# Optimization experiments

Measured on AMD Instinct MI355X. Metric: run time of the kernel, lower is better.

The kernel has to match this reference:

```python
import jax, jax.numpy as jnp
import numpy as np

BN_EPS = 1e-5


def _conv2d(x, w, b, pad):
    # x: [B,C,H,W], w: [O,I,kh,kw] (OIHW)
    y = jax.lax.conv_general_dilated(
        x, w, window_strides=(1, 1), padding=[(pad, pad), (pad, pad)],
        dimension_numbers=('NCHW', 'OIHW', 'NCHW'))
    return y + b[None, :, None, None]


def setup_inputs() -> dict:
    key = jax.random.key(0)
    ks = jax.random.split(key, 4)
    B, C, D, H, W = 8, 256, 1, 64, 64
    dm = 256
    x = jax.random.normal(ks[0], (B, C, D, H, W), dtype=jnp.float32)
    wq = jax.random.normal(ks[1], (dm, dm, 1, 1), dtype=jnp.float32) * 0.05
    bq = jnp.zeros((dm,), jnp.float32)
    wkv = jax.random.normal(ks[2], (2 * dm, dm, 3, 3), dtype=jnp.float32) * 0.05
    bkv = jnp.zeros((2 * dm,), jnp.float32)
    gamma = jnp.ones((dm,), jnp.float32)
    beta = jnp.zeros((dm,), jnp.float32)
    return {"x": x, "wq": wq, "bq": bq, "wkv": wkv, "bkv": bkv,
            "gamma": gamma, "beta": beta}


def reference(x, wq, bq, wkv, bkv, gamma, beta):
    B = x.shape[0]
    H, W = x.shape[-2], x.shape[-1]
    xc = x.reshape(B, -1, H, W)            # 'b c d h w -> b (c d) h w'
    dm = xc.shape[1]
    q = jax.nn.relu(_conv2d(xc, wq, bq, 0))       # [B,dm,H,W]
    kv = jax.nn.relu(_conv2d(xc, wkv, bkv, 1))    # [B,2dm,H,W]
    k, v = jnp.split(kv, 2, axis=1)

    def tok(t):  # 'b c x y -> b (x y) c'
        return t.transpose(0, 2, 3, 1).reshape(B, H * W, dm)

    qt, kt, vt = tok(q), tok(k), tok(v)
    sim = jnp.einsum('bid,bjd->bij', qt, kt)       # [B,N,N]
    A = jax.nn.softmax(sim / jnp.sqrt(jnp.float32(dm)), axis=-1)
    r = jnp.einsum('bij,bjd->bid', A, vt)          # [B,N,dm]
    r = r.reshape(B, H, W, dm).transpose(0, 3, 1, 2)  # 'b (x y) c -> b c x y'
    y = r + xc
    # BatchNorm2d, training mode: batch stats over (B,H,W), biased variance
    mean = jnp.mean(y, axis=(0, 2, 3), keepdims=True)
    var = jnp.var(y, axis=(0, 2, 3), keepdims=True)
    out = (y - mean) * jax.lax.rsqrt(var + BN_EPS)
    out = out * gamma[None, :, None, None] + beta[None, :, None, None]
    return out
```

## Files before the change

kernel.cpp:

```cpp
#include <hip/hip_runtime.h>


typedef __attribute__((ext_vector_type(8))) short bf16x8;
typedef __attribute__((ext_vector_type(4))) float f32x4;
typedef __attribute__((ext_vector_type(8))) unsigned short u16x8;

__device__ inline unsigned short f2bf(float f) {
  union { float f; unsigned u; } c; c.f = f;
  unsigned u = c.u;
  return (unsigned short)((u + 0x7fffu + ((u >> 16) & 1u)) >> 16);
}

__device__ inline unsigned cvtpk(float lo, float hi) {
  unsigned r;
  asm("v_cvt_pk_bf16_f32 %0, %1, %2" : "=v"(r) : "v"(lo), "v"(hi));
  return r;
}

__device__ inline void dma16(const void* g, void* l) {
  __builtin_amdgcn_global_load_lds(
      (const __attribute__((address_space(1))) unsigned int*)g,
      (__attribute__((address_space(3))) unsigned int*)l, 16, 0, 0);
}

__global__ __launch_bounds__(256) void k_xt(
    const float* __restrict__ x, ushort* __restrict__ xt)
{
  const int b = blockIdx.z, ci0 = blockIdx.y * 64, gx = blockIdx.x;
  const int t = threadIdx.x;
  ushort* img = xt + (size_t)b * 4224 * 256;
  if (gx >= 64) {
    int r0 = (gx == 64) ? 0 : 4160;
#pragma unroll
    for (int k = 0; k < 2; ++k) {
      int idx = t + k * 256;
      int r = idx >> 3, u = idx & 7;
      u16x8 z = (u16x8)0;
      *(u16x8*)&img[(size_t)(r0 + r) * 256 + ci0 + u * 8] = z;
    }
    return;
  }
  const int n0 = gx * 64;
  __shared__ ushort tl[64][65];
  {
    const float* xb = x + ((size_t)b * 256 + ci0) * 4096 + n0;
    int i = t >> 2, j0 = (t & 3) * 16;
#pragma unroll
    for (int jj = 0; jj < 16; jj += 4) {
      float4 v = *(const float4*)&xb[(size_t)i * 4096 + j0 + jj];
      tl[j0 + jj + 0][i] = f2bf(v.x);
      tl[j0 + jj + 1][i] = f2bf(v.y);
      tl[j0 + jj + 2][i] = f2bf(v.z);
      tl[j0 + jj + 3][i] = f2bf(v.w);
    }
  }
  __syncthreads();
  {
    int j = t >> 3, u = t & 7;
#pragma unroll
    for (int k = 0; k < 2; ++k) {
      int jr = j + k * 32;
      ushort tmp[8];
#pragma unroll
      for (int e = 0; e < 8; ++e) tmp[e] = tl[jr][u * 8 + e];
      *(u16x8*)&img[(size_t)(64 + n0 + jr) * 256 + ci0 + u * 8] = *(u16x8*)tmp;
    }
  }
}

__global__ __launch_bounds__(256) void k_wprep(
    const float* __restrict__ w, ushort* __restrict__ wt, int ntaps, int nco)
{
  const int co = blockIdx.x;
  const int t = threadIdx.x;
  __shared__ float ws[2304];
  const int tot = 256 * ntaps;
  for (int i = t; i < tot; i += 256) ws[i] = w[(size_t)co * tot + i];
  __syncthreads();
  for (int tap = 0; tap < ntaps; ++tap)
    wt[((size_t)tap * nco + co) * 256 + t] = f2bf(ws[t * ntaps + tap]);
}

__global__ __launch_bounds__(256, 2) void k_conv(
    const ushort* __restrict__ xt, const ushort* __restrict__ wt,
    const float* __restrict__ bias, ushort* __restrict__ outT,
    ushort* __restrict__ outV, int ntaps, int nco, float oscale)
{
  extern __shared__ unsigned char smem[];
  ushort* As = (ushort*)smem;
  ushort* Bs = (ushort*)(smem + 20640);
  __shared__ float bias_s[256];

  const int t = threadIdx.x, lane = t & 63, wv = t >> 6;
  const int wm = wv >> 1, wn = wv & 1;
  const int qc = lane & 15, grp = lane >> 4;
  const int b = blockIdx.z, n0 = blockIdx.x * 128, co0 = blockIdx.y * 256;
  const bool nchw = (outV != nullptr) && (blockIdx.y == 1);
  const ushort* img = xt + (size_t)b * 4224 * 256 + (size_t)64 * 256;

  bias_s[t] = bias[co0 + t];

  f32x4 acc[4][8];
#pragma unroll
  for (int mi = 0; mi < 4; ++mi)
#pragma unroll
    for (int ni = 0; ni < 8; ++ni) acc[mi][ni] = f32x4{0.f, 0.f, 0.f, 0.f};

  for (int c8 = 0; c8 < 8; ++c8) {
    const int ci0 = c8 * 32;
    __syncthreads();
#pragma unroll
    for (int k = 0; k < 5; ++k) {
      int idx = t + k * 256;
      if (idx < 1032) {
        int r = idx >> 2, u = idx & 3;
        int n = n0 + r - 65;
        n = min(max(n, -64), 4159);
        u16x8 v = *(const u16x8*)&img[(size_t)n * 256 + ci0 + u * 8];
        *(u16x8*)&As[r * 40 + u * 8] = v;
      }
    }
    for (int tap = 0; tap < ntaps; ++tap) {
      const int dy = (ntaps == 9) ? (tap / 3 - 1) : 0;
      const int dx = (ntaps == 9) ? (tap % 3 - 1) : 0;
      const int off = dy * 64 + dx;
      __syncthreads();
      const ushort* wrow = wt + ((size_t)tap * nco + co0) * 256 + ci0;
#pragma unroll
      for (int k = 0; k < 4; ++k) {
        int idx = t + k * 256;
        int r = idx >> 2, u = idx & 3;
        *(u16x8*)&Bs[r * 40 + u * 8] = *(const u16x8*)&wrow[(size_t)r * 256 + u * 8];
      }
      __syncthreads();
      bf16x8 bf[8];
#pragma unroll
      for (int ni = 0; ni < 8; ++ni)
        bf[ni] = *(const bf16x8*)&Bs[(wn * 128 + ni * 16 + qc) * 40 + grp * 8];
#pragma unroll
      for (int mi = 0; mi < 4; ++mi) {
        int ar = wm * 64 + mi * 16 + qc + off + 65;
        bf16x8 af = *(const bf16x8*)&As[ar * 40 + grp * 8];
        if (dx < 0 && mi == 0 && qc == 0)  af = (bf16x8)0;
        if (dx > 0 && mi == 3 && qc == 15) af = (bf16x8)0;
#pragma unroll
        for (int ni = 0; ni < 8; ++ni)
          acc[mi][ni] = __builtin_amdgcn_mfma_f32_16x16x32_bf16(af, bf[ni], acc[mi][ni], 0, 0, 0);
      }
    }
  }

  __syncthreads();
  if (!nchw) {
    ushort (*olds)[264] = (ushort(*)[264])smem;
#pragma unroll
    for (int mi = 0; mi < 4; ++mi) {
      int p = wm * 64 + mi * 16 + grp * 4;
#pragma unroll
      for (int ni = 0; ni < 8; ++ni) {
        int c = wn * 128 + ni * 16 + qc;
        float bv = bias_s[c];
#pragma unroll
        for (int r = 0; r < 4; ++r)
          olds[p + r][c] = f2bf(fmaxf(acc[mi][ni][r] + bv, 0.f) * oscale);
      }
    }
    __syncthreads();
    ushort* dst = outT + ((size_t)b * 4096 + n0) * 256;
#pragma unroll
    for (int k = 0; k < 16; ++k) {
      int idx = t + k * 256;
      int r = idx >> 5, u = idx & 31;
      *(u16x8*)&dst[(size_t)r * 256 + u * 8] = *(const u16x8*)&olds[r][u * 8];
    }
  } else {
    ushort (*oldsT)[136] = (ushort(*)[136])smem;
#pragma unroll
    for (int mi = 0; mi < 4; ++mi) {
      int p = wm * 64 + mi * 16 + grp * 4;
#pragma unroll
      for (int ni = 0; ni < 8; ++ni) {
        int c = wn * 128 + ni * 16 + qc;
        float bv = bias_s[c];
        ushort4 pk;
        pk.x = f2bf(fmaxf(acc[mi][ni][0] + bv, 0.f) * oscale);
        pk.y = f2bf(fmaxf(acc[mi][ni][1] + bv, 0.f) * oscale);
        pk.z = f2bf(fmaxf(acc[mi][ni][2] + bv, 0.f) * oscale);
        pk.w = f2bf(fmaxf(acc[mi][ni][3] + bv, 0.f) * oscale);
        *(ushort4*)&oldsT[c][p] = pk;
      }
    }
    __syncthreads();
    ushort* dst = outV + (size_t)b * 256 * 4096 + n0;
#pragma unroll
    for (int k = 0; k < 16; ++k) {
      int idx = t + k * 256;
      int c = idx >> 4, u = idx & 15;
      *(u16x8*)&dst[(size_t)c * 4096 + u * 8] = *(const u16x8*)&oldsT[c][u * 8];
    }
  }
}

__global__ __launch_bounds__(512, 2) void k_attn(
    const ushort* __restrict__ q_t, const ushort* __restrict__ k_t,
    const ushort* __restrict__ v_t, const float* __restrict__ x,
    float* __restrict__ y)
{
  extern __shared__ unsigned char smem[];
  ushort* kbf0 = (ushort*)smem;
  ushort* kbf1 = (ushort*)(smem + 32768);
  ushort* vbf0 = (ushort*)(smem + 65536);
  ushort* vbf1 = (ushort*)(smem + 98304);
  ushort* pl   = (ushort*)(smem + 131072);

  const int tid = threadIdx.x, lane = tid & 63, w = tid >> 6;
  const int grp = lane >> 4, qc = lane & 15, xr = qc & 7;
  const int b = blockIdx.y, q0 = blockIdx.x * 128;
  const int wbase = tid & ~63;

  int offk[4], offv[4];
#pragma unroll
  for (int k = 0; k < 4; ++k) {
    int i = k * 512 + tid;
    int j = i >> 5, s = i & 31;
    offk[k] = j * 256 + ((s ^ (j & 7)) << 3);
    int d = i >> 3, s2 = i & 7;
    offv[k] = d * 4096 + ((s2 ^ (d & 7)) << 3);
  }
  const ushort* kT = k_t + (size_t)b * 4096 * 256;
  const ushort* vT = v_t + (size_t)b * 256 * 4096;

  bf16x8 qf[8];
  {
    const ushort* qrow = q_t + ((size_t)b * 4096 + q0 + w * 16 + qc) * 256;
#pragma unroll
    for (int dc = 0; dc < 8; ++dc)
      qf[dc] = *(const bf16x8*)&qrow[dc * 32 + grp * 8];
  }

  f32x4 o[16];
#pragma unroll
  for (int dt = 0; dt < 16; ++dt) o[dt] = f32x4{0.f, 0.f, 0.f, 0.f};
  float m_run = -1e30f, lp = 0.f;

  auto stage = [&](const ushort* kp, const ushort* vp, ushort* kb, ushort* vb) {
#pragma unroll
    for (int k = 0; k < 4; ++k)
      dma16(kp + offk[k], kb + (size_t)(k * 512 + wbase) * 8);
#pragma unroll
    for (int k = 0; k < 4; ++k)
      dma16(vp + offv[k], vb + (size_t)(k * 512 + wbase) * 8);
  };

  stage(kT, vT, kbf0, vbf0);
  kT += 16384; vT += 64;
  asm volatile("s_waitcnt vmcnt(0)" ::: "memory");
  __syncthreads();

  ushort* prow = pl + (size_t)(w * 16 + qc) * 64;
  int po[4], pslot[2];
#pragma unroll
  for (int kt = 0; kt < 4; ++kt)
    po[kt] = (((2 * kt + (grp >> 1)) ^ xr) << 3) + ((grp & 1) << 2);
#pragma unroll
  for (int kc = 0; kc < 2; ++kc)
    pslot[kc] = ((kc * 4 + grp) ^ xr) << 3;

  for (int t = 0; t < 64; ++t) {
    ushort* kb = (t & 1) ? kbf1 : kbf0;
    ushort* vb = (t & 1) ? vbf1 : vbf0;
    if (t < 63) {
      stage(kT, vT, (t & 1) ? kbf0 : kbf1, (t & 1) ? vbf0 : vbf1);
      kT += 16384; vT += 64;
    }

    f32x4 st[4];
    __builtin_amdgcn_s_setprio(1);
#pragma unroll
    for (int kt = 0; kt < 4; ++kt) {
      f32x4 a = f32x4{0.f, 0.f, 0.f, 0.f};
      const int row = (kt * 16 + qc) * 256;
#pragma unroll
      for (int dc = 0; dc < 8; ++dc) {
        bf16x8 ka = *(const bf16x8*)&kb[row + (((dc * 4 + grp) ^ xr) << 3)];
        a = __builtin_amdgcn_mfma_f32_16x16x32_bf16(ka, qf[dc], a, 0, 0, 0);
      }
      st[kt] = a;
    }
    __builtin_amdgcn_s_setprio(0);

    float pmax = fmaxf(
        fmaxf(fmaxf(st[0][0], st[0][1]), fmaxf(st[0][2], st[0][3])),
        fmaxf(fmaxf(st[1][0], st[1][1]), fmaxf(st[1][2], st[1][3])));
    pmax = fmaxf(pmax, fmaxf(
        fmaxf(fmaxf(st[2][0], st[2][1]), fmaxf(st[2][2], st[2][3])),
        fmaxf(fmaxf(st[3][0], st[3][1]), fmaxf(st[3][2], st[3][3]))));
    pmax = fmaxf(pmax, __shfl_xor(pmax, 16));
    pmax = fmaxf(pmax, __shfl_xor(pmax, 32));
    if (pmax - m_run > 11.5f) {
      float mn = fmaxf(m_run, pmax);
      float al = exp2f(m_run - mn);
      m_run = mn; lp *= al;
#pragma unroll
      for (int dt = 0; dt < 16; ++dt) {
        o[dt][0] *= al; o[dt][1] *= al; o[dt][2] *= al; o[dt][3] *= al;
      }
    }
#pragma unroll
    for (int kt = 0; kt < 4; ++kt) {
      float p0 = exp2f(st[kt][0] - m_run);
      float p1 = exp2f(st[kt][1] - m_run);
      float p2 = exp2f(st[kt][2] - m_run);
      float p3 = exp2f(st[kt][3] - m_run);
      lp += (p0 + p1) + (p2 + p3);
      uint2 pk = { cvtpk(p0, p1), cvtpk(p2, p3) };
      *(uint2*)&prow[po[kt]] = pk;
    }

    bf16x8 pb0 = *(const bf16x8*)&prow[pslot[0]];
    bf16x8 pb1 = *(const bf16x8*)&prow[pslot[1]];
    __builtin_amdgcn_s_setprio(1);
#pragma unroll
    for (int dt = 0; dt < 16; ++dt) {
      const int vrow = (dt * 16 + qc) * 64;
      bf16x8 va0 = *(const bf16x8*)&vb[vrow + pslot[0]];
      bf16x8 va1 = *(const bf16x8*)&vb[vrow + pslot[1]];
      o[dt] = __builtin_amdgcn_mfma_f32_16x16x32_bf16(va0, pb0, o[dt], 0, 0, 0);
      o[dt] = __builtin_amdgcn_mfma_f32_16x16x32_bf16(va1, pb1, o[dt], 0, 0, 0);
    }
    __builtin_amdgcn_s_setprio(0);

    asm volatile("s_waitcnt vmcnt(0)" ::: "memory");
    __syncthreads();
  }

  lp += __shfl_xor(lp, 16);
  lp += __shfl_xor(lp, 32);
  float inv = 1.f / lp;

  float (*obuf)[132] = (float(*)[132])smem;
#pragma unroll
  for (int dt = 0; dt < 16; ++dt)
#pragma unroll
    for (int r = 0; r < 4; ++r)
      obuf[dt * 16 + grp * 4 + r][w * 16 + qc] = o[dt][r] * inv;
  __syncthreads();

  const float* xb = x + (size_t)b * 256 * 4096 + q0;
  float*       yb = y + (size_t)b * 256 * 4096 + q0;
  for (int i = tid; i < 8192; i += 512) {
    int c = i >> 5, f4 = (i & 31) << 2;
    float4 xr4 = *(const float4*)&xb[(size_t)c * 4096 + f4];
    float4 rv = *(const float4*)&obuf[c][f4];
    rv.x += xr4.x; rv.y += xr4.y; rv.z += xr4.z; rv.w += xr4.w;
    *(float4*)&yb[(size_t)c * 4096 + f4] = rv;
  }
}

__global__ __launch_bounds__(256) void k_bnstats(
    const float* __restrict__ y, const float* __restrict__ gamma,
    const float* __restrict__ beta, float* __restrict__ scale,
    float* __restrict__ shift)
{
  const int c = blockIdx.x;
  const int tid = threadIdx.x;
  double s1 = 0.0, s2 = 0.0;
  for (int i = tid; i < 32768; i += 256) {
    int bb = i >> 12, n = i & 4095;
    float v = y[((size_t)bb * 256 + c) * 4096 + n];
    s1 += (double)v;
    s2 += (double)v * (double)v;
  }
  __shared__ double r1[256], r2[256];
  r1[tid] = s1; r2[tid] = s2;
  __syncthreads();
  for (int st = 128; st; st >>= 1) {
    if (tid < st) { r1[tid] += r1[tid + st]; r2[tid] += r2[tid + st]; }
    __syncthreads();
  }
  if (tid == 0) {
    double mean = r1[0] / 32768.0;
    double var  = r2[0] / 32768.0 - mean * mean;
    double inv  = 1.0 / sqrt(var + 1e-5);
    double gg = (double)gamma[c];
    scale[c] = (float)(gg * inv);
    shift[c] = (float)((double)beta[c] - mean * gg * inv);
  }
}

__global__ __launch_bounds__(256) void k_bnapply(
    float* __restrict__ y, const float* __restrict__ scale,
    const float* __restrict__ shift)
{
  const int total4 = 8 * 256 * 1024;
  for (int i = blockIdx.x * 256 + threadIdx.x; i < total4; i += gridDim.x * 256) {
    int c = (i >> 10) & 255;
    float sc = scale[c], sh = shift[c];
    float4 v = ((const float4*)y)[i];
    v.x = fmaf(v.x, sc, sh);
    v.y = fmaf(v.y, sc, sh);
    v.z = fmaf(v.z, sc, sh);
    v.w = fmaf(v.w, sc, sh);
    ((float4*)y)[i] = v;
  }
}

extern "C" void kernel_launch(void* const* d_in, const int* in_sizes, int n_in,
                              void* d_out, int out_size, void* d_ws, size_t ws_size,
                              hipStream_t stream) {
  const float* x     = (const float*)d_in[0];
  const float* wq    = (const float*)d_in[1];
  const float* bq    = (const float*)d_in[2];
  const float* wkv   = (const float*)d_in[3];
  const float* bkv   = (const float*)d_in[4];
  const float* gamma = (const float*)d_in[5];
  const float* beta  = (const float*)d_in[6];
  float* out = (float*)d_out;

  ushort* xt  = (ushort*)d_ws;
  ushort* wt3 = xt  + (size_t)8650752;
  ushort* wt1 = wt3 + (size_t)1179648;
  ushort* q_t = wt1 + (size_t)65536;
  ushort* k_t = q_t + (size_t)8388608;
  ushort* v_t = k_t + (size_t)8388608;
  float* scale = (float*)(v_t + (size_t)8388608);
  float* shift = scale + 256;

  k_xt<<<dim3(66, 4, 8), 256, 0, stream>>>(x, xt);
  k_wprep<<<dim3(512), 256, 0, stream>>>(wkv, wt3, 9, 512);
  k_wprep<<<dim3(256), 256, 0, stream>>>(wq, wt1, 1, 256);

  const int conv_smem = 69632;
  hipFuncSetAttribute(reinterpret_cast<const void*>(k_conv),
                      hipFuncAttributeMaxDynamicSharedMemorySize, conv_smem);
  k_conv<<<dim3(32, 1, 8), 256, conv_smem, stream>>>(
      xt, wt1, bq, q_t, nullptr, 1, 256, 0.0625f * 1.44269504f);
  k_conv<<<dim3(32, 2, 8), 256, conv_smem, stream>>>(
      xt, wt3, bkv, k_t, v_t, 9, 512, 1.0f);

  const int attn_smem = 147456;
  hipFuncSetAttribute(reinterpret_cast<const void*>(k_attn),
                      hipFuncAttributeMaxDynamicSharedMemorySize, attn_smem);
  k_attn<<<dim3(32, 8), 512, attn_smem, stream>>>(q_t, k_t, v_t, x, out);

  k_bnstats<<<dim3(256), 256, 0, stream>>>(out, gamma, beta, scale, shift);
  k_bnapply<<<dim3(2048), 256, 0, stream>>>(out, scale, shift);
}
```

Measured before the change: 343.0 us.

## Fuse BatchNorm statistics into attention epilogue and batch LDS operand loads

The attention epilogue now accumulates per-channel sum and sum-of-squares into shared memory with atomics, then adds them into a global stat buffer. This replaces the separate stats kernel that re-read the whole output, leaving a tiny finalize kernel. Separately, K and V operand loads from LDS are hoisted into register arrays, with V double-buffered across groups, so MFMAs are not stalled on each load. Stats move from double to float with the E[x^2]-mean^2 formula, which risks precision loss, and the extra registers may pressure occupancy.

```diff
diff --git a/kernel.cpp b/kernel.cpp
--- a/kernel.cpp
+++ b/kernel.cpp
@@ -204,7 +204,7 @@
 __global__ __launch_bounds__(512, 2) void k_attn(
     const ushort* __restrict__ q_t, const ushort* __restrict__ k_t,
     const ushort* __restrict__ v_t, const float* __restrict__ x,
-    float* __restrict__ y)
+    float* __restrict__ y, float* __restrict__ gstat)
 {
   extern __shared__ unsigned char smem[];
   ushort* kbf0 = (ushort*)smem;
@@ -278,13 +278,15 @@
     __builtin_amdgcn_s_setprio(1);
 #pragma unroll
     for (int kt = 0; kt < 4; ++kt) {
+      const int row = (kt * 16 + qc) * 256;
+      bf16x8 ka8[8];
+#pragma unroll
+      for (int dc = 0; dc < 8; ++dc)
+        ka8[dc] = *(const bf16x8*)&kb[row + (((dc * 4 + grp) ^ xr) << 3)];
       f32x4 a = f32x4{0.f, 0.f, 0.f, 0.f};
-      const int row = (kt * 16 + qc) * 256;
-#pragma unroll
-      for (int dc = 0; dc < 8; ++dc) {
-        bf16x8 ka = *(const bf16x8*)&kb[row + (((dc * 4 + grp) ^ xr) << 3)];
-        a = __builtin_amdgcn_mfma_f32_16x16x32_bf16(ka, qf[dc], a, 0, 0, 0);
-      }
+#pragma unroll
+      for (int dc = 0; dc < 8; ++dc)
+        a = __builtin_amdgcn_mfma_f32_16x16x32_bf16(ka8[dc], qf[dc], a, 0, 0, 0);
       st[kt] = a;
     }
     __builtin_amdgcn_s_setprio(0);
@@ -319,14 +321,30 @@
 
     bf16x8 pb0 = *(const bf16x8*)&prow[pslot[0]];
     bf16x8 pb1 = *(const bf16x8*)&prow[pslot[1]];
+    bf16x8 vaA[8], vaB[8];
+#pragma unroll
+    for (int j = 0; j < 8; ++j) {
+      int dt = j >> 1;
+      vaA[j] = *(const bf16x8*)&vb[(dt * 16 + qc) * 64 + pslot[j & 1]];
+    }
     __builtin_amdgcn_s_setprio(1);
 #pragma unroll
-    for (int dt = 0; dt < 16; ++dt) {
-      const int vrow = (dt * 16 + qc) * 64;
-      bf16x8 va0 = *(const bf16x8*)&vb[vrow + pslot[0]];
-      bf16x8 va1 = *(const bf16x8*)&vb[vrow + pslot[1]];
-      o[dt] = __builtin_amdgcn_mfma_f32_16x16x32_bf16(va0, pb0, o[dt], 0, 0, 0);
-      o[dt] = __builtin_amdgcn_mfma_f32_16x16x32_bf16(va1, pb1, o[dt], 0, 0, 0);
+    for (int bt = 0; bt < 4; ++bt) {
+      const bf16x8* cur = (bt & 1) ? vaB : vaA;
+      bf16x8* nxt = (bt & 1) ? vaA : vaB;
+      if (bt < 3) {
+#pragma unroll
+        for (int j = 0; j < 8; ++j) {
+          int dt = (bt + 1) * 4 + (j >> 1);
+          nxt[j] = *(const bf16x8*)&vb[(dt * 16 + qc) * 64 + pslot[j & 1]];
+        }
+      }
+#pragma unroll
+      for (int j2 = 0; j2 < 4; ++j2) {
+        int dt = bt * 4 + j2;
+        o[dt] = __builtin_amdgcn_mfma_f32_16x16x32_bf16(cur[2 * j2],     pb0, o[dt], 0, 0, 0);
+        o[dt] = __builtin_amdgcn_mfma_f32_16x16x32_bf16(cur[2 * j2 + 1], pb1, o[dt], 0, 0, 0);
+      }
     }
     __builtin_amdgcn_s_setprio(0);
 
@@ -339,6 +357,8 @@
   float inv = 1.f / lp;
 
   float (*obuf)[132] = (float(*)[132])smem;
+  float* bnacc = (float*)(smem + 135168);
+  bnacc[tid] = 0.f;
 #pragma unroll
   for (int dt = 0; dt < 16; ++dt)
 #pragma unroll
@@ -354,38 +374,30 @@
     float4 rv = *(const float4*)&obuf[c][f4];
     rv.x += xr4.x; rv.y += xr4.y; rv.z += xr4.z; rv.w += xr4.w;
     *(float4*)&yb[(size_t)c * 4096 + f4] = rv;
-  }
-}
-
-__global__ __launch_bounds__(256) void k_bnstats(
-    const float* __restrict__ y, const float* __restrict__ gamma,
+    float ls1 = (rv.x + rv.y) + (rv.z + rv.w);
+    float ls2 = (rv.x * rv.x + rv.y * rv.y) + (rv.z * rv.z + rv.w * rv.w);
+    atomicAdd(&bnacc[c], ls1);
+    atomicAdd(&bnacc[256 + c], ls2);
+  }
+  __syncthreads();
+  if (tid < 256) {
+    atomicAdd(&gstat[tid], bnacc[tid]);
+    atomicAdd(&gstat[256 + tid], bnacc[256 + tid]);
+  }
+}
+
+__global__ __launch_bounds__(256) void k_bnfin(
+    const float* __restrict__ gstat, const float* __restrict__ gamma,
     const float* __restrict__ beta, float* __restrict__ scale,
     float* __restrict__ shift)
 {
-  const int c = blockIdx.x;
-  const int tid = threadIdx.x;
-  double s1 = 0.0, s2 = 0.0;
-  for (int i = tid; i < 32768; i += 256) {
-    int bb = i >> 12, n = i & 4095;
-    float v = y[((size_t)bb * 256 + c) * 4096 + n];
-    s1 += (double)v;
-    s2 += (double)v * (double)v;
-  }
-  __shared__ double r1[256], r2[256];
-  r1[tid] = s1; r2[tid] = s2;
-  __syncthreads();
-  for (int st = 128; st; st >>= 1) {
-    if (tid < st) { r1[tid] += r1[tid + st]; r2[tid] += r2[tid + st]; }
-    __syncthreads();
-  }
-  if (tid == 0) {
-    double mean = r1[0] / 32768.0;
-    double var  = r2[0] / 32768.0 - mean * mean;
-    double inv  = 1.0 / sqrt(var + 1e-5);
-    double gg = (double)gamma[c];
-    scale[c] = (float)(gg * inv);
-    shift[c] = (float)((double)beta[c] - mean * gg * inv);
-  }
+  const int c = threadIdx.x;
+  float mean = gstat[c] * (1.f / 32768.f);
+  float var  = gstat[256 + c] * (1.f / 32768.f) - mean * mean;
+  float inv  = rsqrtf(var + 1e-5f);
+  float g = gamma[c] * inv;
+  scale[c] = g;
+  shift[c] = beta[c] - mean * g;
 }
 
 __global__ __launch_bounds__(256) void k_bnapply(
@@ -425,6 +437,9 @@
   ushort* v_t = k_t + (size_t)8388608;
   float* scale = (float*)(v_t + (size_t)8388608);
   float* shift = scale + 256;
+  float* gstat = shift + 256;
+
+  hipMemsetAsync(gstat, 0, 2048, stream);
 
   k_xt<<<dim3(66, 4, 8), 256, 0, stream>>>(x, xt);
   k_wprep<<<dim3(512), 256, 0, stream>>>(wkv, wt3, 9, 512);
@@ -441,8 +456,8 @@
   const int attn_smem = 147456;
   hipFuncSetAttribute(reinterpret_cast<const void*>(k_attn),
                       hipFuncAttributeMaxDynamicSharedMemorySize, attn_smem);
-  k_attn<<<dim3(32, 8), 512, attn_smem, stream>>>(q_t, k_t, v_t, x, out);
-
-  k_bnstats<<<dim3(256), 256, 0, stream>>>(out, gamma, beta, scale, shift);
+  k_attn<<<dim3(32, 8), 512, attn_smem, stream>>>(q_t, k_t, v_t, x, out, gstat);
+
+  k_bnfin<<<dim3(1), 256, 0, stream>>>(gstat, gamma, beta, scale, shift);
   k_bnapply<<<dim3(2048), 256, 0, stream>>>(out, scale, shift);
 }
```

After: 332.6 us. 3.0% less time.
